# Kernel optimization log

Hardware: AMD Instinct MI355X
Metric: run time of the kernel (lower is better)

The kernel has to match this reference:

```python
import jax, jax.numpy as jnp
import numpy as np

S_IN = 32      # input spatial size
KSZ = 3        # kernel size
STRIDE = 1
S_OUT = (S_IN - KSZ) // STRIDE + 1   # 30
C_IN = 16      # input capsule types
C_OUT = 32     # output capsule types
ROUTINGS = 3
EPS = 1e-7     # K.epsilon()


def _child_parent_map(size_in, size_out, kernel_size):
    # For each parent position, the flat indices of its kernel_size^2 children.
    cpm = np.zeros((size_out ** 2, kernel_size ** 2), dtype=np.int32)
    for p in range(size_out ** 2):
        idx = []
        for kr in range(kernel_size):
            start = kr * size_in + p % size_out + (p // size_out) * size_in
            idx.extend(range(start, start + kernel_size))
        cpm[p] = idx
    return cpm

_CPM = jnp.asarray(_child_parent_map(S_IN, S_OUT, KSZ))  # [S_OUT^2, KSZ^2]


def setup_inputs() -> dict:
    key = jax.random.key(0)
    k1, k2, k3, k4, k5 = jax.random.split(key, 5)
    return {
        "input_act": jax.random.uniform(k1, (S_IN, S_IN, C_IN, 1), dtype=jnp.float32),
        "input_pose": jax.random.normal(k2, (S_IN, S_IN, C_IN, 4, 4), dtype=jnp.float32),
        "transformation_weights": jax.random.normal(k3, (1, KSZ * KSZ * C_IN, C_OUT, 4, 4), dtype=jnp.float32) * 0.1,
        "beta_a": jax.random.normal(k4, (1, 1, C_OUT), dtype=jnp.float32),
        "beta_v": jax.random.normal(k5, (1, 1, C_OUT, 1), dtype=jnp.float32),
    }


def reference(input_act, input_pose, transformation_weights, beta_a, beta_v):
    P = S_OUT ** 2                 # parent positions
    N = KSZ * KSZ * C_IN           # children per parent

    pose = input_pose.reshape(S_IN ** 2, C_IN, 4, 4)
    act = input_act.reshape(S_IN ** 2, C_IN, 1)

    # gather children per parent position (irregular gather via child_parent_map)
    pose_f = pose[_CPM].reshape(P, N, 4, 4)        # [P, N, 4, 4]
    act_f = act[_CPM].reshape(P, N, 1, 1)          # [P, N, 1, 1] (broadcasts over C_OUT)

    W = transformation_weights[0]                  # [N, C_OUT, 4, 4]
    # votes[p,n,c,i,j] = sum_k pose_f[p,n,i,k] * W[n,c,k,j] (avoids K.tile materialization)
    votes = jnp.einsum('pnik,nckj->pncij', pose_f, W).reshape(P, N, C_OUT, 16)

    rr = jnp.full((P, N, C_OUT, 1), 1.0 / C_OUT, dtype=votes.dtype)

    out_act = None
    means = None
    for i in range(ROUTINGS):
        lambd = 0.01 * (1.0 - 0.95 ** i)
        # ---- M step ----
        rs = jnp.sum(rr, axis=1, keepdims=True)                              # [P,1,C,1]
        means = jnp.sum(rr * votes, axis=1, keepdims=True) / rs              # [P,1,C,16]
        var = jnp.sum(rr * jnp.square(votes - means), axis=1, keepdims=True) / rs
        std = jnp.sqrt(var)                                                  # [P,1,C,16]
        costs = beta_v + jnp.log(std + EPS) * rs                             # [P,1,C,16]
        out_act = jax.nn.sigmoid(lambd * (beta_a - jnp.sum(costs, axis=-1)))[..., None]  # [P,1,C,1]
        if i < ROUTINGS - 1:
            # ---- E step ----
            prob_exp = -jnp.sum(jnp.square(votes - means) / (2.0 * jnp.square(std)),
                                axis=-1, keepdims=True)                      # [P,N,C,1]
            prob_main = -jnp.sum(jnp.log(std + EPS), axis=-1, keepdims=True)  # [P,1,C,1]
            zz = jnp.log(out_act + EPS) + prob_main + prob_exp
            rr = jax.nn.softmax(zz, axis=0)                                   # softmax over parent axis, as in source

    out_act = out_act.reshape(S_OUT, S_OUT, C_OUT, 1)
    out_pose = means.reshape(S_OUT, S_OUT, C_OUT, 4, 4)
    return (out_act, out_pose)
```

## Files before the change

### kernel.cpp

```cpp
#include <hip/hip_runtime.h>


#define S_IN   32
#define S_OUT  30
#define PP     (S_OUT * S_OUT)
#define NN     144
#define NREP   16
#define PLSZ   (NN * 32)
#define EPSF   1e-7f
#define CLAMPA 80.0f

#define LOADW(dst, n_) do {                                              \
    const float4* _wp = (const float4*)&W[((n_) * 32 + c) * 16];         \
    float4 _w0 = _wp[0], _w1 = _wp[1], _w2 = _wp[2], _w3 = _wp[3];       \
    dst[0] = _w0.x; dst[1] = _w0.y; dst[2] = _w0.z; dst[3] = _w0.w;      \
    dst[4] = _w1.x; dst[5] = _w1.y; dst[6] = _w1.z; dst[7] = _w1.w;      \
    dst[8] = _w2.x; dst[9] = _w2.y; dst[10] = _w2.z; dst[11] = _w2.w;    \
    dst[12] = _w3.x; dst[13] = _w3.y; dst[14] = _w3.z; dst[15] = _w3.w;  \
} while (0)

#define LOADPO(dst, n_) do {                                             \
    const float4* _pp = (const float4*)&pose_s[(n_) * 16];               \
    float4 _p0 = _pp[0], _p1 = _pp[1], _p2 = _pp[2], _p3 = _pp[3];       \
    dst[0] = _p0.x; dst[1] = _p0.y; dst[2] = _p0.z; dst[3] = _p0.w;      \
    dst[4] = _p1.x; dst[5] = _p1.y; dst[6] = _p1.z; dst[7] = _p1.w;      \
    dst[8] = _p2.x; dst[9] = _p2.y; dst[10] = _p2.z; dst[11] = _p2.w;    \
    dst[12] = _p3.x; dst[13] = _p3.y; dst[14] = _p3.z; dst[15] = _p3.w;  \
} while (0)

#define VOTES(v_, po_, w_) do {                                          \
    _Pragma("unroll")                                                    \
    for (int _i = 0; _i < 4; ++_i) {                                     \
        float _p0 = po_[_i*4+0], _p1 = po_[_i*4+1];                      \
        float _p2 = po_[_i*4+2], _p3 = po_[_i*4+3];                      \
        _Pragma("unroll")                                                \
        for (int _j = 0; _j < 4; ++_j)                                   \
            v_[_i*4+_j] = fmaf(_p0, w_[_j], fmaf(_p1, w_[4+_j],          \
                          fmaf(_p2, w_[8+_j], _p3 * w_[12+_j])));        \
    }                                                                    \
} while (0)

template <bool FIRST, bool LAST>
__global__ __launch_bounds__(512, 4) void me_kernel(
    const float* __restrict__ pose,
    const float* __restrict__ W,
    const float* __restrict__ beta_a,
    const float* __restrict__ beta_v,
    const float* __restrict__ csC,
    float* __restrict__ csW,
    float* __restrict__ meanw,
    float* __restrict__ i2vw,
    float* __restrict__ basew,
    float* __restrict__ out,
    float lambd)
{
    const int p = blockIdx.x;
    const int t = threadIdx.x;
    const int c = t & 31;
    const int slot = t >> 5;
    const int wave = t >> 6;
    const int rep = p & (NREP - 1);

    __shared__ float pose_s[NN * 16];
    __shared__ float red[33 * 8 * 32];
    __shared__ float mean_s[16 * 32];
    __shared__ float i2v_s[16 * 32];
    __shared__ float base_s[32];
    __shared__ float lg[4 * 32];

    const int prow = p / S_OUT, pcol = p % S_OUT;
    {
        const float4* pose4 = (const float4*)pose;
        float4* ps4 = (float4*)pose_s;
        for (int idx = t; idx < 576; idx += 512) {
            int kk = idx >> 6;
            int child = (prow + kk / 3) * S_IN + (pcol + kk % 3);
            ps4[idx] = pose4[child * 64 + (idx & 63)];
        }
    }

    float mn[16], iv[16], base = 0.f;
    if (!FIRST) {
        const float4* m4 = (const float4*)&meanw[(p * 32 + c) * 16];
        const float4* v4 = (const float4*)&i2vw[(p * 32 + c) * 16];
#pragma unroll
        for (int q = 0; q < 4; ++q) {
            float4 a = m4[q], b = v4[q];
            mn[q * 4 + 0] = a.x; mn[q * 4 + 1] = a.y; mn[q * 4 + 2] = a.z; mn[q * 4 + 3] = a.w;
            iv[q * 4 + 0] = b.x; iv[q * 4 + 1] = b.y; iv[q * 4 + 2] = b.z; iv[q * 4 + 3] = b.w;
        }
        base = basew[p * 32 + c];
    }
    __syncthreads();

    float rsum = 0.f;
    float s1[16], s2[16];
#pragma unroll
    for (int q = 0; q < 16; ++q) { s1[q] = 0.f; s2[q] = 0.f; }

    float w[16];
    LOADW(w, slot);
    float cs = 1.f;
    if (!FIRST) cs = csC[slot * 32 + c];

    for (int k = 0; k < 9; ++k) {
        const int n = (k << 4) + slot;
        float po[16];
        LOADPO(po, n);
        float v[16];
        VOTES(v, po, w);
        float cs_next = cs;
        if (k < 8) {
            LOADW(w, n + 16);
            if (!FIRST) cs_next = csC[(n + 16) * 32 + c];
        }
        if (FIRST) {
#pragma unroll
            for (int q = 0; q < 16; ++q) {
                s1[q] += v[q];
                s2[q] = fmaf(v[q], v[q], s2[q]);
            }
        } else {
            float pe = 0.f;
#pragma unroll
            for (int q = 0; q < 16; ++q) {
                float d = v[q] - mn[q];
                pe = fmaf(d * d, iv[q], pe);
            }
            float r = __expf(fminf(base - pe, CLAMPA)) * __builtin_amdgcn_rcpf(cs);
#pragma unroll
            for (int q = 0; q < 16; ++q) {
                s1[q] = fmaf(r, v[q], s1[q]);
                float rv = r * v[q];
                s2[q] = fmaf(rv, v[q], s2[q]);
            }
            rsum += r;
        }
        cs = cs_next;
    }

#pragma unroll
    for (int q = 0; q < 16; ++q) {
        s1[q] += __shfl_xor(s1[q], 32);
        s2[q] += __shfl_xor(s2[q], 32);
    }
    rsum += __shfl_xor(rsum, 32);

    if ((t & 32) == 0) {
#pragma unroll
        for (int q = 0; q < 16; ++q) {
            red[(q * 8 + wave) * 32 + c] = s1[q];
            red[((16 + q) * 8 + wave) * 32 + c] = s2[q];
        }
        red[(32 * 8 + wave) * 32 + c] = rsum;
    }
    __syncthreads();

    if (t < 128) {
        const int qq = t >> 5, cl = t & 31;
        float rs, inv_rs;
        if (FIRST) {
            rs = 4.5f;
            inv_rs = 1.0f / 144.0f;
        } else {
            rs = 0.f;
#pragma unroll
            for (int w8 = 0; w8 < 8; ++w8) rs += red[(32 * 8 + w8) * 32 + cl];
            inv_rs = 1.0f / rs;
        }
        float lsum = 0.f;
        float mq[4], vq[4];
#pragma unroll
        for (int u = 0; u < 4; ++u) {
            const int q = qq * 4 + u;
            float a1 = 0.f, a2 = 0.f;
#pragma unroll
            for (int w8 = 0; w8 < 8; ++w8) {
                a1 += red[(q * 8 + w8) * 32 + cl];
                a2 += red[((16 + q) * 8 + w8) * 32 + cl];
            }
            float m = a1 * inv_rs;
            float var = fmaxf(a2 * inv_rs - m * m, 1e-30f);
            float sd = __builtin_sqrtf(var);
            mq[u] = m;
            vq[u] = 0.5f / var;
            lsum += __logf(sd + EPSF);
            mean_s[q * 32 + cl] = m;
            i2v_s[q * 32 + cl] = vq[u];
        }
        lg[qq * 32 + cl] = lsum;
        float4 mv; mv.x = mq[0]; mv.y = mq[1]; mv.z = mq[2]; mv.w = mq[3];
        if (LAST) {
            ((float4*)(out + PP * 32))[(p * 32 + cl) * 4 + qq] = mv;
        } else {
            float4 vv; vv.x = vq[0]; vv.y = vq[1]; vv.z = vq[2]; vv.w = vq[3];
            ((float4*)meanw)[(p * 32 + cl) * 4 + qq] = mv;
            ((float4*)i2vw)[(p * 32 + cl) * 4 + qq] = vv;
        }
    }
    __syncthreads();

    if (t < 32) {
        float rs;
        if (FIRST) {
            rs = 4.5f;
        } else {
            rs = 0.f;
#pragma unroll
            for (int w8 = 0; w8 < 8; ++w8) rs += red[(32 * 8 + w8) * 32 + c];
        }
        float lsum = lg[c] + lg[32 + c] + lg[64 + c] + lg[96 + c];
        float sumcosts = 16.f * beta_v[c] + rs * lsum;
        float a = 1.0f / (1.0f + __expf(-(lambd * (beta_a[c] - sumcosts))));
        if (LAST) {
            out[p * 32 + c] = a;
        } else {
            float b = __logf(a + EPSF) - lsum;
            basew[p * 32 + c] = b;
            base_s[c] = b;
        }
    }

    if (!LAST) {
        __syncthreads();
        float tbase = base_s[c];
#pragma unroll
        for (int q = 0; q < 16; ++q) {
            mn[q] = mean_s[q * 32 + c];
            iv[q] = i2v_s[q * 32 + c];
        }
        LOADW(w, slot);
        float* csp = csW + rep * PLSZ;
        for (int k = 0; k < 9; ++k) {
            const int n = (k << 4) + slot;
            float po[16];
            LOADPO(po, n);
            float v[16];
            VOTES(v, po, w);
            if (k < 8) LOADW(w, n + 16);
            float pe = 0.f;
#pragma unroll
            for (int q = 0; q < 16; ++q) {
                float d = v[q] - mn[q];
                pe = fmaf(d * d, iv[q], pe);
            }
            float e = __expf(fminf(tbase - pe, CLAMPA));
            atomicAdd(&csp[n * 32 + c], e);
        }
    }
}

__global__ __launch_bounds__(256) void collapse_kernel(
    const float* __restrict__ planes, float* __restrict__ csum)
{
    const int idx = blockIdx.x * 256 + threadIdx.x;
    if (idx >= PLSZ) return;
    float s0 = 0.f, s1 = 0.f, s2 = 0.f, s3 = 0.f;
#pragma unroll
    for (int r = 0; r < NREP; r += 4) {
        s0 += planes[(r + 0) * PLSZ + idx];
        s1 += planes[(r + 1) * PLSZ + idx];
        s2 += planes[(r + 2) * PLSZ + idx];
        s3 += planes[(r + 3) * PLSZ + idx];
    }
    csum[idx] = (s0 + s1) + (s2 + s3);
}

extern "C" void kernel_launch(void* const* d_in, const int* in_sizes, int n_in,
                              void* d_out, int out_size, void* d_ws, size_t ws_size,
                              hipStream_t stream) {
    const float* pose   = (const float*)d_in[1];
    const float* W      = (const float*)d_in[2];
    const float* beta_a = (const float*)d_in[3];
    const float* beta_v = (const float*)d_in[4];
    float* out = (float*)d_out;
    float* ws = (float*)d_ws;

    float* meanw   = ws;
    float* i2vw    = meanw + PP * 32 * 16;
    float* basew   = i2vw + PP * 32 * 16;
    float* planes0 = basew + PP * 32;
    float* planes1 = planes0 + NREP * PLSZ;
    float* csum0   = planes1 + NREP * PLSZ;
    float* csum1   = csum0 + PLSZ;

    const float lambd0 = 0.0f;
    const float lambd1 = 0.01f * (1.0f - 0.95f);
    const float lambd2 = 0.01f * (1.0f - 0.95f * 0.95f);

    const int cg = (PLSZ + 255) / 256;

    hipMemsetAsync(planes0, 0, 2 * NREP * PLSZ * sizeof(float), stream);

    me_kernel<true, false><<<PP, 512, 0, stream>>>(
        pose, W, beta_a, beta_v, csum0, planes0, meanw, i2vw, basew, out, lambd0);
    collapse_kernel<<<cg, 256, 0, stream>>>(planes0, csum0);
    me_kernel<false, false><<<PP, 512, 0, stream>>>(
        pose, W, beta_a, beta_v, csum0, planes1, meanw, i2vw, basew, out, lambd1);
    collapse_kernel<<<cg, 256, 0, stream>>>(planes1, csum1);
    me_kernel<false, true><<<PP, 512, 0, stream>>>(
        pose, W, beta_a, beta_v, csum1, nullptr, meanw, i2vw, basew, out, lambd2);
}
```

Measured before the change: 122.7 us.

## Process two horizontally adjacent parents per block to share weight loads

Each block now handles two neighbouring parent positions (pA, pA+1). It loads a 3x4 child window into shared memory and reuses each transformation-weight register load for both parents' votes. The aim is to halve per-parent weight traffic and block count and to cut launch and sync overhead per parent. In exchange, register pressure roughly doubles: launch bounds drop to 2 blocks per SM, loops are fully unrolled, and the stats and base phases run serially for the two parents.

```diff
diff --git a/kernel.cpp b/kernel.cpp
--- a/kernel.cpp
+++ b/kernel.cpp
@@ -7,6 +7,7 @@
 #define NN     144
 #define NREP   16
 #define PLSZ   (NN * 32)
+#define NBLK   (PP / 2)
 #define EPSF   1e-7f
 #define CLAMPA 80.0f
 
@@ -19,8 +20,8 @@
     dst[12] = _w3.x; dst[13] = _w3.y; dst[14] = _w3.z; dst[15] = _w3.w;  \
 } while (0)
 
-#define LOADPO(dst, n_) do {                                             \
-    const float4* _pp = (const float4*)&pose_s[(n_) * 16];               \
+#define LOADPO(dst, row_) do {                                           \
+    const float4* _pp = (const float4*)&pose_s[(row_) * 16];             \
     float4 _p0 = _pp[0], _p1 = _pp[1], _p2 = _pp[2], _p3 = _pp[3];       \
     dst[0] = _p0.x; dst[1] = _p0.y; dst[2] = _p0.z; dst[3] = _p0.w;      \
     dst[4] = _p1.x; dst[5] = _p1.y; dst[6] = _p1.z; dst[7] = _p1.w;      \
@@ -40,8 +41,118 @@
     }                                                                    \
 } while (0)
 
+#define PE(pe_, v_, mn_, iv_) float pe_;                                 \
+    do {                                                                 \
+        float _a = 0.f, _b = 0.f;                                        \
+        _Pragma("unroll")                                                \
+        for (int _q = 0; _q < 16; _q += 2) {                             \
+            float _d0 = v_[_q] - mn_[_q];                                \
+            float _d1 = v_[_q+1] - mn_[_q+1];                            \
+            _a = fmaf(_d0 * _d0, iv_[_q], _a);                           \
+            _b = fmaf(_d1 * _d1, iv_[_q+1], _b);                         \
+        }                                                                \
+        pe_ = _a + _b;                                                   \
+    } while (0)
+
+#define LOADSTATS(mn_, iv_, p_) do {                                     \
+    const float4* _m4 = (const float4*)&meanw[((p_) * 32 + c) * 16];     \
+    const float4* _v4 = (const float4*)&i2vw[((p_) * 32 + c) * 16];      \
+    _Pragma("unroll")                                                    \
+    for (int _q = 0; _q < 4; ++_q) {                                     \
+        float4 _a = _m4[_q], _b = _v4[_q];                               \
+        mn_[_q*4+0] = _a.x; mn_[_q*4+1] = _a.y;                          \
+        mn_[_q*4+2] = _a.z; mn_[_q*4+3] = _a.w;                          \
+        iv_[_q*4+0] = _b.x; iv_[_q*4+1] = _b.y;                          \
+        iv_[_q*4+2] = _b.z; iv_[_q*4+3] = _b.w;                          \
+    }                                                                    \
+} while (0)
+
+#define WRITE_RED(S1, S2, RS) do {                                       \
+    if ((t & 32) == 0) {                                                 \
+        _Pragma("unroll")                                                \
+        for (int q = 0; q < 16; ++q) {                                   \
+            red[(q * 8 + wave) * 32 + c] = S1[q];                        \
+            red[((16 + q) * 8 + wave) * 32 + c] = S2[q];                 \
+        }                                                                \
+        red[(32 * 8 + wave) * 32 + c] = RS;                              \
+    }                                                                    \
+} while (0)
+
+__constant__ int UA_TAB[9] = {0, 1, 2, 4, 5, 6, 8, 9, 10};
+
 template <bool FIRST, bool LAST>
-__global__ __launch_bounds__(512, 4) void me_kernel(
+__device__ __forceinline__ void stats_phase(
+    const float* __restrict__ red, float* lg, float* rs_s,
+    float* mean_sp, float* i2v_sp,
+    float* __restrict__ meanw, float* __restrict__ i2vw,
+    float* __restrict__ out, int p, int t)
+{
+    if (t < 128) {
+        const int qq = t >> 5, cl = t & 31;
+        float rs, inv_rs;
+        if (FIRST) { rs = 4.5f; inv_rs = 1.0f / 144.0f; }
+        else {
+            rs = 0.f;
+#pragma unroll
+            for (int w8 = 0; w8 < 8; ++w8) rs += red[(32 * 8 + w8) * 32 + cl];
+            inv_rs = 1.0f / rs;
+        }
+        if (qq == 0) rs_s[cl] = rs;
+        float lsum = 0.f;
+        float mq[4], vq[4];
+#pragma unroll
+        for (int u = 0; u < 4; ++u) {
+            const int q = qq * 4 + u;
+            float a1 = 0.f, a2 = 0.f;
+#pragma unroll
+            for (int w8 = 0; w8 < 8; ++w8) {
+                a1 += red[(q * 8 + w8) * 32 + cl];
+                a2 += red[((16 + q) * 8 + w8) * 32 + cl];
+            }
+            float m = a1 * inv_rs;
+            float var = fmaxf(a2 * inv_rs - m * m, 1e-30f);
+            float sd = __builtin_sqrtf(var);
+            mq[u] = m; vq[u] = 0.5f / var;
+            lsum += __logf(sd + EPSF);
+            mean_sp[q * 32 + cl] = m;
+            i2v_sp[q * 32 + cl] = vq[u];
+        }
+        lg[qq * 32 + cl] = lsum;
+        float4 mv; mv.x = mq[0]; mv.y = mq[1]; mv.z = mq[2]; mv.w = mq[3];
+        if (LAST) {
+            ((float4*)(out + PP * 32))[(p * 32 + cl) * 4 + qq] = mv;
+        } else {
+            float4 vv; vv.x = vq[0]; vv.y = vq[1]; vv.z = vq[2]; vv.w = vq[3];
+            ((float4*)meanw)[(p * 32 + cl) * 4 + qq] = mv;
+            ((float4*)i2vw)[(p * 32 + cl) * 4 + qq] = vv;
+        }
+    }
+}
+
+template <bool FIRST, bool LAST>
+__device__ __forceinline__ void base_phase(
+    const float* lg, const float* rs_s, float* base_sp,
+    const float* __restrict__ beta_a, const float* __restrict__ beta_v,
+    float* __restrict__ basew, float* __restrict__ out, int p, int t, float lambd)
+{
+    if (t < 32) {
+        const int c = t;
+        float rs = FIRST ? 4.5f : rs_s[c];
+        float lsum = lg[c] + lg[32 + c] + lg[64 + c] + lg[96 + c];
+        float sumcosts = 16.f * beta_v[c] + rs * lsum;
+        float a = 1.0f / (1.0f + __expf(-(lambd * (beta_a[c] - sumcosts))));
+        if (LAST) {
+            out[p * 32 + c] = a;
+        } else {
+            float b = __logf(a + EPSF) - lsum;
+            basew[p * 32 + c] = b;
+            base_sp[c] = b;
+        }
+    }
+}
+
+template <bool FIRST, bool LAST>
+__global__ __launch_bounds__(512, 2) void me_kernel(
     const float* __restrict__ pose,
     const float* __restrict__ W,
     const float* __restrict__ beta_a,
@@ -54,198 +165,146 @@
     float* __restrict__ out,
     float lambd)
 {
-    const int p = blockIdx.x;
+    const int b = blockIdx.x;
+    const int pA = 2 * b, pB = 2 * b + 1;
     const int t = threadIdx.x;
     const int c = t & 31;
     const int slot = t >> 5;
     const int wave = t >> 6;
-    const int rep = p & (NREP - 1);
-
-    __shared__ float pose_s[NN * 16];
+
+    __shared__ float pose_s[12 * 16 * 16];
     __shared__ float red[33 * 8 * 32];
-    __shared__ float mean_s[16 * 32];
-    __shared__ float i2v_s[16 * 32];
-    __shared__ float base_s[32];
+    __shared__ float mean_s[2][16 * 32];
+    __shared__ float i2v_s[2][16 * 32];
+    __shared__ float base_s[2][32];
+    __shared__ float rs_s[2][32];
     __shared__ float lg[4 * 32];
 
-    const int prow = p / S_OUT, pcol = p % S_OUT;
+    const int rowA = pA / S_OUT, colA = pA % S_OUT;
     {
         const float4* pose4 = (const float4*)pose;
         float4* ps4 = (float4*)pose_s;
-        for (int idx = t; idx < 576; idx += 512) {
-            int kk = idx >> 6;
-            int child = (prow + kk / 3) * S_IN + (pcol + kk % 3);
+        for (int idx = t; idx < 768; idx += 512) {
+            int u = idx >> 6;
+            int child = (rowA + (u >> 2)) * S_IN + (colA + (u & 3));
             ps4[idx] = pose4[child * 64 + (idx & 63)];
         }
     }
 
-    float mn[16], iv[16], base = 0.f;
+    float mnA[16], ivA[16], mnB[16], ivB[16], baseA = 0.f, baseB = 0.f;
     if (!FIRST) {
-        const float4* m4 = (const float4*)&meanw[(p * 32 + c) * 16];
-        const float4* v4 = (const float4*)&i2vw[(p * 32 + c) * 16];
-#pragma unroll
-        for (int q = 0; q < 4; ++q) {
-            float4 a = m4[q], b = v4[q];
-            mn[q * 4 + 0] = a.x; mn[q * 4 + 1] = a.y; mn[q * 4 + 2] = a.z; mn[q * 4 + 3] = a.w;
-            iv[q * 4 + 0] = b.x; iv[q * 4 + 1] = b.y; iv[q * 4 + 2] = b.z; iv[q * 4 + 3] = b.w;
-        }
-        base = basew[p * 32 + c];
-    }
-    __syncthreads();
-
-    float rsum = 0.f;
-    float s1[16], s2[16];
-#pragma unroll
-    for (int q = 0; q < 16; ++q) { s1[q] = 0.f; s2[q] = 0.f; }
+        LOADSTATS(mnA, ivA, pA);
+        LOADSTATS(mnB, ivB, pB);
+        baseA = basew[pA * 32 + c];
+        baseB = basew[pB * 32 + c];
+    }
+    __syncthreads();
+
+    float rsumA = 0.f, rsumB = 0.f;
+    float s1A[16], s2A[16], s1B[16], s2B[16];
+#pragma unroll
+    for (int q = 0; q < 16; ++q) {
+        s1A[q] = 0.f; s2A[q] = 0.f; s1B[q] = 0.f; s2B[q] = 0.f;
+    }
 
     float w[16];
     LOADW(w, slot);
     float cs = 1.f;
     if (!FIRST) cs = csC[slot * 32 + c];
 
+#pragma unroll
     for (int k = 0; k < 9; ++k) {
         const int n = (k << 4) + slot;
-        float po[16];
-        LOADPO(po, n);
-        float v[16];
-        VOTES(v, po, w);
-        float cs_next = cs;
+        const int uA = UA_TAB[k];
+        float poA[16]; LOADPO(poA, uA * 16 + slot);
+        float vA[16];  VOTES(vA, poA, w);
+        float poB[16]; LOADPO(poB, (uA + 1) * 16 + slot);
+        float vB[16];  VOTES(vB, poB, w);
+        const float csq = cs;
         if (k < 8) {
             LOADW(w, n + 16);
-            if (!FIRST) cs_next = csC[(n + 16) * 32 + c];
+            if (!FIRST) cs = csC[(n + 16) * 32 + c];
         }
         if (FIRST) {
 #pragma unroll
             for (int q = 0; q < 16; ++q) {
-                s1[q] += v[q];
-                s2[q] = fmaf(v[q], v[q], s2[q]);
+                s1A[q] += vA[q];
+                s2A[q] = fmaf(vA[q], vA[q], s2A[q]);
+                s1B[q] += vB[q];
+                s2B[q] = fmaf(vB[q], vB[q], s2B[q]);
             }
         } else {
-            float pe = 0.f;
+            PE(peA, vA, mnA, ivA);
+            PE(peB, vB, mnB, ivB);
+            const float inv_cs = __builtin_amdgcn_rcpf(csq);
+            float rA = __expf(fminf(baseA - peA, CLAMPA)) * inv_cs;
+            float rB = __expf(fminf(baseB - peB, CLAMPA)) * inv_cs;
 #pragma unroll
             for (int q = 0; q < 16; ++q) {
-                float d = v[q] - mn[q];
-                pe = fmaf(d * d, iv[q], pe);
+                s1A[q] = fmaf(rA, vA[q], s1A[q]);
+                s2A[q] = fmaf(rA * vA[q], vA[q], s2A[q]);
+                s1B[q] = fmaf(rB, vB[q], s1B[q]);
+                s2B[q] = fmaf(rB * vB[q], vB[q], s2B[q]);
             }
-            float r = __expf(fminf(base - pe, CLAMPA)) * __builtin_amdgcn_rcpf(cs);
-#pragma unroll
-            for (int q = 0; q < 16; ++q) {
-                s1[q] = fmaf(r, v[q], s1[q]);
-                float rv = r * v[q];
-                s2[q] = fmaf(rv, v[q], s2[q]);
-            }
-            rsum += r;
-        }
-        cs = cs_next;
+            rsumA += rA;
+            rsumB += rB;
+        }
     }
 
 #pragma unroll
     for (int q = 0; q < 16; ++q) {
-        s1[q] += __shfl_xor(s1[q], 32);
-        s2[q] += __shfl_xor(s2[q], 32);
-    }
-    rsum += __shfl_xor(rsum, 32);
-
-    if ((t & 32) == 0) {
-#pragma unroll
-        for (int q = 0; q < 16; ++q) {
-            red[(q * 8 + wave) * 32 + c] = s1[q];
-            red[((16 + q) * 8 + wave) * 32 + c] = s2[q];
-        }
-        red[(32 * 8 + wave) * 32 + c] = rsum;
-    }
-    __syncthreads();
-
-    if (t < 128) {
-        const int qq = t >> 5, cl = t & 31;
-        float rs, inv_rs;
-        if (FIRST) {
-            rs = 4.5f;
-            inv_rs = 1.0f / 144.0f;
-        } else {
-            rs = 0.f;
-#pragma unroll
-            for (int w8 = 0; w8 < 8; ++w8) rs += red[(32 * 8 + w8) * 32 + cl];
-            inv_rs = 1.0f / rs;
-        }
-        float lsum = 0.f;
-        float mq[4], vq[4];
-#pragma unroll
-        for (int u = 0; u < 4; ++u) {
-            const int q = qq * 4 + u;
-            float a1 = 0.f, a2 = 0.f;
-#pragma unroll
-            for (int w8 = 0; w8 < 8; ++w8) {
-                a1 += red[(q * 8 + w8) * 32 + cl];
-                a2 += red[((16 + q) * 8 + w8) * 32 + cl];
-            }
-            float m = a1 * inv_rs;
-            float var = fmaxf(a2 * inv_rs - m * m, 1e-30f);
-            float sd = __builtin_sqrtf(var);
-            mq[u] = m;
-            vq[u] = 0.5f / var;
-            lsum += __logf(sd + EPSF);
-            mean_s[q * 32 + cl] = m;
-            i2v_s[q * 32 + cl] = vq[u];
-        }
-        lg[qq * 32 + cl] = lsum;
-        float4 mv; mv.x = mq[0]; mv.y = mq[1]; mv.z = mq[2]; mv.w = mq[3];
-        if (LAST) {
-            ((float4*)(out + PP * 32))[(p * 32 + cl) * 4 + qq] = mv;
-        } else {
-            float4 vv; vv.x = vq[0]; vv.y = vq[1]; vv.z = vq[2]; vv.w = vq[3];
-            ((float4*)meanw)[(p * 32 + cl) * 4 + qq] = mv;
-            ((float4*)i2vw)[(p * 32 + cl) * 4 + qq] = vv;
-        }
-    }
-    __syncthreads();
-
-    if (t < 32) {
-        float rs;
-        if (FIRST) {
-            rs = 4.5f;
-        } else {
-            rs = 0.f;
-#pragma unroll
-            for (int w8 = 0; w8 < 8; ++w8) rs += red[(32 * 8 + w8) * 32 + c];
-        }
-        float lsum = lg[c] + lg[32 + c] + lg[64 + c] + lg[96 + c];
-        float sumcosts = 16.f * beta_v[c] + rs * lsum;
-        float a = 1.0f / (1.0f + __expf(-(lambd * (beta_a[c] - sumcosts))));
-        if (LAST) {
-            out[p * 32 + c] = a;
-        } else {
-            float b = __logf(a + EPSF) - lsum;
-            basew[p * 32 + c] = b;
-            base_s[c] = b;
-        }
-    }
+        s1A[q] += __shfl_xor(s1A[q], 32);
+        s2A[q] += __shfl_xor(s2A[q], 32);
+        s1B[q] += __shfl_xor(s1B[q], 32);
+        s2B[q] += __shfl_xor(s2B[q], 32);
+    }
+    rsumA += __shfl_xor(rsumA, 32);
+    rsumB += __shfl_xor(rsumB, 32);
+
+    WRITE_RED(s1A, s2A, rsumA);
+    __syncthreads();
+    stats_phase<FIRST, LAST>(red, lg, rs_s[0], mean_s[0], i2v_s[0],
+                             meanw, i2vw, out, pA, t);
+    __syncthreads();
+    base_phase<FIRST, LAST>(lg, rs_s[0], base_s[0], beta_a, beta_v,
+                            basew, out, pA, t, lambd);
+    WRITE_RED(s1B, s2B, rsumB);
+    __syncthreads();
+    stats_phase<FIRST, LAST>(red, lg, rs_s[1], mean_s[1], i2v_s[1],
+                             meanw, i2vw, out, pB, t);
+    __syncthreads();
+    base_phase<FIRST, LAST>(lg, rs_s[1], base_s[1], beta_a, beta_v,
+                            basew, out, pB, t, lambd);
 
     if (!LAST) {
         __syncthreads();
-        float tbase = base_s[c];
 #pragma unroll
         for (int q = 0; q < 16; ++q) {
-            mn[q] = mean_s[q * 32 + c];
-            iv[q] = i2v_s[q * 32 + c];
-        }
+            mnA[q] = mean_s[0][q * 32 + c];
+            ivA[q] = i2v_s[0][q * 32 + c];
+            mnB[q] = mean_s[1][q * 32 + c];
+            ivB[q] = i2v_s[1][q * 32 + c];
+        }
+        const float bA = base_s[0][c];
+        const float bB = base_s[1][c];
         LOADW(w, slot);
-        float* csp = csW + rep * PLSZ;
+        float* cspA = csW + (pA & (NREP - 1)) * PLSZ;
+        float* cspB = csW + (pB & (NREP - 1)) * PLSZ;
+#pragma unroll
         for (int k = 0; k < 9; ++k) {
             const int n = (k << 4) + slot;
-            float po[16];
-            LOADPO(po, n);
-            float v[16];
-            VOTES(v, po, w);
+            const int uA = UA_TAB[k];
+            float poA[16]; LOADPO(poA, uA * 16 + slot);
+            float vA[16];  VOTES(vA, poA, w);
+            float poB[16]; LOADPO(poB, (uA + 1) * 16 + slot);
+            float vB[16];  VOTES(vB, poB, w);
             if (k < 8) LOADW(w, n + 16);
-            float pe = 0.f;
-#pragma unroll
-            for (int q = 0; q < 16; ++q) {
-                float d = v[q] - mn[q];
-                pe = fmaf(d * d, iv[q], pe);
-            }
-            float e = __expf(fminf(tbase - pe, CLAMPA));
-            atomicAdd(&csp[n * 32 + c], e);
+            PE(peA, vA, mnA, ivA);
+            PE(peB, vB, mnB, ivB);
+            float eA = __expf(fminf(bA - peA, CLAMPA));
+            float eB = __expf(fminf(bB - peB, CLAMPA));
+            atomicAdd(&cspA[n * 32 + c], eA);
+            atomicAdd(&cspB[n * 32 + c], eB);
         }
     }
 }
@@ -292,12 +351,12 @@
 
     hipMemsetAsync(planes0, 0, 2 * NREP * PLSZ * sizeof(float), stream);
 
-    me_kernel<true, false><<<PP, 512, 0, stream>>>(
+    me_kernel<true, false><<<NBLK, 512, 0, stream>>>(
         pose, W, beta_a, beta_v, csum0, planes0, meanw, i2vw, basew, out, lambd0);
     collapse_kernel<<<cg, 256, 0, stream>>>(planes0, csum0);
-    me_kernel<false, false><<<PP, 512, 0, stream>>>(
+    me_kernel<false, false><<<NBLK, 512, 0, stream>>>(
         pose, W, beta_a, beta_v, csum0, planes1, meanw, i2vw, basew, out, lambd1);
     collapse_kernel<<<cg, 256, 0, stream>>>(planes1, csum1);
-    me_kernel<false, true><<<PP, 512, 0, stream>>>(
+    me_kernel<false, true><<<NBLK, 512, 0, stream>>>(
         pose, W, beta_a, beta_v, csum1, nullptr, meanw, i2vw, basew, out, lambd2);
 }
```

New measurement: 129.4 us. 5.5% more time.

## Expand Gaussian exponent algebraically and split reduction to cut shared memory

Applied to the files above, without the earlier changes.

Rewrites the per-vote exponent sum (v-m)^2*iv as v*(iv*v - 2*iv*m) plus a constant folded into the base term. This trims the subtraction per component and uses two independent accumulators. The block reduction now handles s1 and s2 in two passes over a smaller shared buffer, with all 512 threads finishing one component each. The k loops are fully unrolled. The changes aim to lower ALU work, shared-memory footprint and occupancy pressure, at the cost of extra barriers, scalar global stores and possible loss of precision from cancellation in the expanded quadratic.

```diff
diff --git a/kernel.cpp b/kernel.cpp
--- a/kernel.cpp
+++ b/kernel.cpp
@@ -39,6 +39,19 @@
                           fmaf(_p2, w_[8+_j], _p3 * w_[12+_j])));        \
     }                                                                    \
 } while (0)
+
+#define PEQ(pe_, v_, iv_, m2b_) float pe_;                               \
+    do {                                                                 \
+        float _a = 0.f, _b = 0.f;                                        \
+        _Pragma("unroll")                                                \
+        for (int _q = 0; _q < 16; _q += 2) {                             \
+            float _t0 = fmaf(iv_[_q], v_[_q], m2b_[_q]);                 \
+            float _t1 = fmaf(iv_[_q+1], v_[_q+1], m2b_[_q+1]);           \
+            _a = fmaf(v_[_q], _t0, _a);                                  \
+            _b = fmaf(v_[_q+1], _t1, _b);                                \
+        }                                                                \
+        pe_ = _a + _b;                                                   \
+    } while (0)
 
 template <bool FIRST, bool LAST>
 __global__ __launch_bounds__(512, 4) void me_kernel(
@@ -59,14 +72,16 @@
     const int c = t & 31;
     const int slot = t >> 5;
     const int wave = t >> 6;
-    const int rep = p & (NREP - 1);
 
     __shared__ float pose_s[NN * 16];
-    __shared__ float red[33 * 8 * 32];
+    __shared__ float red[16 * 8 * 32];
+    __shared__ float rsum_s[8 * 32];
     __shared__ float mean_s[16 * 32];
-    __shared__ float i2v_s[16 * 32];
-    __shared__ float base_s[32];
-    __shared__ float lg[4 * 32];
+    __shared__ float iv_s[16 * 32];
+    __shared__ float m2b_s[16 * 32];
+    __shared__ float logstd_s[16 * 32];
+    __shared__ float rs_s[32];
+    __shared__ float bstar_s[32];
 
     const int prow = p / S_OUT, pcol = p % S_OUT;
     {
@@ -79,17 +94,26 @@
         }
     }
 
-    float mn[16], iv[16], base = 0.f;
+    float iv[16], m2b[16], bstar = 0.f;
     if (!FIRST) {
+        float cst = 0.f;
         const float4* m4 = (const float4*)&meanw[(p * 32 + c) * 16];
         const float4* v4 = (const float4*)&i2vw[(p * 32 + c) * 16];
 #pragma unroll
-        for (int q = 0; q < 4; ++q) {
-            float4 a = m4[q], b = v4[q];
-            mn[q * 4 + 0] = a.x; mn[q * 4 + 1] = a.y; mn[q * 4 + 2] = a.z; mn[q * 4 + 3] = a.w;
-            iv[q * 4 + 0] = b.x; iv[q * 4 + 1] = b.y; iv[q * 4 + 2] = b.z; iv[q * 4 + 3] = b.w;
-        }
-        base = basew[p * 32 + c];
+        for (int q4 = 0; q4 < 4; ++q4) {
+            float4 a = m4[q4], b = v4[q4];
+            float mq[4] = {a.x, a.y, a.z, a.w};
+            float vq[4] = {b.x, b.y, b.z, b.w};
+#pragma unroll
+            for (int u = 0; u < 4; ++u) {
+                int q = q4 * 4 + u;
+                iv[q] = vq[u];
+                float tq = vq[u] * mq[u];
+                m2b[q] = -2.f * tq;
+                cst = fmaf(tq, mq[u], cst);
+            }
+        }
+        bstar = basew[p * 32 + c] - cst;
     }
     __syncthreads();
 
@@ -103,16 +127,17 @@
     float cs = 1.f;
     if (!FIRST) cs = csC[slot * 32 + c];
 
+#pragma unroll
     for (int k = 0; k < 9; ++k) {
         const int n = (k << 4) + slot;
         float po[16];
         LOADPO(po, n);
         float v[16];
         VOTES(v, po, w);
-        float cs_next = cs;
+        const float csq = cs;
         if (k < 8) {
             LOADW(w, n + 16);
-            if (!FIRST) cs_next = csC[(n + 16) * 32 + c];
+            if (!FIRST) cs = csC[(n + 16) * 32 + c];
         }
         if (FIRST) {
 #pragma unroll
@@ -121,22 +146,15 @@
                 s2[q] = fmaf(v[q], v[q], s2[q]);
             }
         } else {
-            float pe = 0.f;
-#pragma unroll
-            for (int q = 0; q < 16; ++q) {
-                float d = v[q] - mn[q];
-                pe = fmaf(d * d, iv[q], pe);
-            }
-            float r = __expf(fminf(base - pe, CLAMPA)) * __builtin_amdgcn_rcpf(cs);
+            PEQ(pe, v, iv, m2b);
+            float r = __expf(fminf(bstar - pe, CLAMPA)) * __builtin_amdgcn_rcpf(csq);
 #pragma unroll
             for (int q = 0; q < 16; ++q) {
                 s1[q] = fmaf(r, v[q], s1[q]);
-                float rv = r * v[q];
-                s2[q] = fmaf(rv, v[q], s2[q]);
+                s2[q] = fmaf(r * v[q], v[q], s2[q]);
             }
             rsum += r;
         }
-        cs = cs_next;
     }
 
 #pragma unroll
@@ -148,68 +166,62 @@
 
     if ((t & 32) == 0) {
 #pragma unroll
-        for (int q = 0; q < 16; ++q) {
-            red[(q * 8 + wave) * 32 + c] = s1[q];
-            red[((16 + q) * 8 + wave) * 32 + c] = s2[q];
-        }
-        red[(32 * 8 + wave) * 32 + c] = rsum;
-    }
-    __syncthreads();
-
-    if (t < 128) {
-        const int qq = t >> 5, cl = t & 31;
+        for (int q = 0; q < 16; ++q) red[(q * 8 + wave) * 32 + c] = s1[q];
+        rsum_s[wave * 32 + c] = rsum;
+    }
+    __syncthreads();
+
+    {
+        const int q = slot;
+        float a1 = 0.f;
+#pragma unroll
+        for (int w8 = 0; w8 < 8; ++w8) a1 += red[(q * 8 + w8) * 32 + c];
         float rs, inv_rs;
-        if (FIRST) {
-            rs = 4.5f;
-            inv_rs = 1.0f / 144.0f;
-        } else {
+        if (FIRST) { rs = 4.5f; inv_rs = 1.0f / 144.0f; }
+        else {
             rs = 0.f;
 #pragma unroll
-            for (int w8 = 0; w8 < 8; ++w8) rs += red[(32 * 8 + w8) * 32 + cl];
+            for (int w8 = 0; w8 < 8; ++w8) rs += rsum_s[w8 * 32 + c];
             inv_rs = 1.0f / rs;
         }
+        float mean = a1 * inv_rs;
+        mean_s[q * 32 + c] = mean;
+        if (q == 0) rs_s[c] = rs;
+        if (LAST) out[PP * 32 + (p * 32 + c) * 16 + q] = mean;
+        else      meanw[(p * 32 + c) * 16 + q] = mean;
+    }
+    __syncthreads();
+
+    if ((t & 32) == 0) {
+#pragma unroll
+        for (int q = 0; q < 16; ++q) red[(q * 8 + wave) * 32 + c] = s2[q];
+    }
+    __syncthreads();
+
+    {
+        const int q = slot;
+        float a2 = 0.f;
+#pragma unroll
+        for (int w8 = 0; w8 < 8; ++w8) a2 += red[(q * 8 + w8) * 32 + c];
+        float inv_rs = FIRST ? (1.0f / 144.0f) : (1.0f / rs_s[c]);
+        float mean = mean_s[q * 32 + c];
+        float var = fmaxf(a2 * inv_rs - mean * mean, 1e-30f);
+        float sd = __builtin_sqrtf(var);
+        logstd_s[q * 32 + c] = __logf(sd + EPSF);
+        if (!LAST) {
+            float ivv = 0.5f / var;
+            iv_s[q * 32 + c] = ivv;
+            m2b_s[q * 32 + c] = -2.f * ivv * mean;
+            i2vw[(p * 32 + c) * 16 + q] = ivv;
+        }
+    }
+    __syncthreads();
+
+    if (t < 32) {
+        float rs = FIRST ? 4.5f : rs_s[c];
         float lsum = 0.f;
-        float mq[4], vq[4];
-#pragma unroll
-        for (int u = 0; u < 4; ++u) {
-            const int q = qq * 4 + u;
-            float a1 = 0.f, a2 = 0.f;
-#pragma unroll
-            for (int w8 = 0; w8 < 8; ++w8) {
-                a1 += red[(q * 8 + w8) * 32 + cl];
-                a2 += red[((16 + q) * 8 + w8) * 32 + cl];
-            }
-            float m = a1 * inv_rs;
-            float var = fmaxf(a2 * inv_rs - m * m, 1e-30f);
-            float sd = __builtin_sqrtf(var);
-            mq[u] = m;
-            vq[u] = 0.5f / var;
-            lsum += __logf(sd + EPSF);
-            mean_s[q * 32 + cl] = m;
-            i2v_s[q * 32 + cl] = vq[u];
-        }
-        lg[qq * 32 + cl] = lsum;
-        float4 mv; mv.x = mq[0]; mv.y = mq[1]; mv.z = mq[2]; mv.w = mq[3];
-        if (LAST) {
-            ((float4*)(out + PP * 32))[(p * 32 + cl) * 4 + qq] = mv;
-        } else {
-            float4 vv; vv.x = vq[0]; vv.y = vq[1]; vv.z = vq[2]; vv.w = vq[3];
-            ((float4*)meanw)[(p * 32 + cl) * 4 + qq] = mv;
-            ((float4*)i2vw)[(p * 32 + cl) * 4 + qq] = vv;
-        }
-    }
-    __syncthreads();
-
-    if (t < 32) {
-        float rs;
-        if (FIRST) {
-            rs = 4.5f;
-        } else {
-            rs = 0.f;
-#pragma unroll
-            for (int w8 = 0; w8 < 8; ++w8) rs += red[(32 * 8 + w8) * 32 + c];
-        }
-        float lsum = lg[c] + lg[32 + c] + lg[64 + c] + lg[96 + c];
+#pragma unroll
+        for (int q = 0; q < 16; ++q) lsum += logstd_s[q * 32 + c];
         float sumcosts = 16.f * beta_v[c] + rs * lsum;
         float a = 1.0f / (1.0f + __expf(-(lambd * (beta_a[c] - sumcosts))));
         if (LAST) {
@@ -217,20 +229,27 @@
         } else {
             float b = __logf(a + EPSF) - lsum;
             basew[p * 32 + c] = b;
-            base_s[c] = b;
+            float cst = 0.f;
+#pragma unroll
+            for (int q = 0; q < 16; ++q) {
+                float m = mean_s[q * 32 + c];
+                cst = fmaf(iv_s[q * 32 + c] * m, m, cst);
+            }
+            bstar_s[c] = b - cst;
         }
     }
 
     if (!LAST) {
         __syncthreads();
-        float tbase = base_s[c];
 #pragma unroll
         for (int q = 0; q < 16; ++q) {
-            mn[q] = mean_s[q * 32 + c];
-            iv[q] = i2v_s[q * 32 + c];
-        }
+            iv[q] = iv_s[q * 32 + c];
+            m2b[q] = m2b_s[q * 32 + c];
+        }
+        const float bst = bstar_s[c];
         LOADW(w, slot);
-        float* csp = csW + rep * PLSZ;
+        float* csp = csW + (p & (NREP - 1)) * PLSZ;
+#pragma unroll
         for (int k = 0; k < 9; ++k) {
             const int n = (k << 4) + slot;
             float po[16];
@@ -238,13 +257,8 @@
             float v[16];
             VOTES(v, po, w);
             if (k < 8) LOADW(w, n + 16);
-            float pe = 0.f;
-#pragma unroll
-            for (int q = 0; q < 16; ++q) {
-                float d = v[q] - mn[q];
-                pe = fmaf(d * d, iv[q], pe);
-            }
-            float e = __expf(fminf(tbase - pe, CLAMPA));
+            PEQ(pe, v, iv, m2b);
+            float e = __expf(fminf(bst - pe, CLAMPA));
             atomicAdd(&csp[n * 32 + c], e);
         }
     }
```

Result: slower. 138.9 us (+13.2%).

## Replace atomic softmax-denominator accumulation with per-parent planes and two-stage reduction

Applied to the files above, without the earlier changes.

Each parent block now writes its exp terms to its own plane with plain stores instead of doing atomicAdd into 16 replicated planes. The planes are then summed by a two-stage reduction (20 chunks, then a final pass), which also removes the memset. This is meant to eliminate atomic contention and the memset, but it writes and reads about 16.6 MB of planes per routing iteration and adds an extra kernel launch. A small register tweak in the cs prefetch is included.

```diff
diff --git a/kernel.cpp b/kernel.cpp
--- a/kernel.cpp
+++ b/kernel.cpp
@@ -5,8 +5,9 @@
 #define S_OUT  30
 #define PP     (S_OUT * S_OUT)
 #define NN     144
-#define NREP   16
 #define PLSZ   (NN * 32)
+#define NCH    20
+#define CHP    (PP / NCH)
 #define EPSF   1e-7f
 #define CLAMPA 80.0f
 
@@ -47,7 +48,7 @@
     const float* __restrict__ beta_a,
     const float* __restrict__ beta_v,
     const float* __restrict__ csC,
-    float* __restrict__ csW,
+    float* __restrict__ planes,
     float* __restrict__ meanw,
     float* __restrict__ i2vw,
     float* __restrict__ basew,
@@ -59,7 +60,6 @@
     const int c = t & 31;
     const int slot = t >> 5;
     const int wave = t >> 6;
-    const int rep = p & (NREP - 1);
 
     __shared__ float pose_s[NN * 16];
     __shared__ float red[33 * 8 * 32];
@@ -109,10 +109,10 @@
         LOADPO(po, n);
         float v[16];
         VOTES(v, po, w);
-        float cs_next = cs;
+        const float csq = cs;
         if (k < 8) {
             LOADW(w, n + 16);
-            if (!FIRST) cs_next = csC[(n + 16) * 32 + c];
+            if (!FIRST) cs = csC[(n + 16) * 32 + c];
         }
         if (FIRST) {
 #pragma unroll
@@ -127,16 +127,14 @@
                 float d = v[q] - mn[q];
                 pe = fmaf(d * d, iv[q], pe);
             }
-            float r = __expf(fminf(base - pe, CLAMPA)) * __builtin_amdgcn_rcpf(cs);
+            float r = __expf(fminf(base - pe, CLAMPA)) * __builtin_amdgcn_rcpf(csq);
 #pragma unroll
             for (int q = 0; q < 16; ++q) {
                 s1[q] = fmaf(r, v[q], s1[q]);
-                float rv = r * v[q];
-                s2[q] = fmaf(rv, v[q], s2[q]);
+                s2[q] = fmaf(r * v[q], v[q], s2[q]);
             }
             rsum += r;
         }
-        cs = cs_next;
     }
 
 #pragma unroll
@@ -230,7 +228,7 @@
             iv[q] = i2v_s[q * 32 + c];
         }
         LOADW(w, slot);
-        float* csp = csW + rep * PLSZ;
+        float* csp = planes + p * PLSZ;
         for (int k = 0; k < 9; ++k) {
             const int n = (k << 4) + slot;
             float po[16];
@@ -245,25 +243,47 @@
                 pe = fmaf(d * d, iv[q], pe);
             }
             float e = __expf(fminf(tbase - pe, CLAMPA));
-            atomicAdd(&csp[n * 32 + c], e);
+            csp[n * 32 + c] = e;
         }
     }
 }
 
-__global__ __launch_bounds__(256) void collapse_kernel(
-    const float* __restrict__ planes, float* __restrict__ csum)
+__global__ __launch_bounds__(256) void collapse_a(
+    const float* __restrict__ planes, float* __restrict__ partial)
+{
+    const int b = blockIdx.x;
+    const int ch = b / 18;
+    const int idx = (b % 18) * 256 + threadIdx.x;
+    const float* src = planes + ch * CHP * PLSZ + idx;
+    float a0 = 0.f, a1 = 0.f, a2 = 0.f, a3 = 0.f;
+#pragma unroll
+    for (int o = 0; o < CHP; o += 4) {
+        if (o + 3 < CHP) {
+            a0 += src[(o + 0) * PLSZ];
+            a1 += src[(o + 1) * PLSZ];
+            a2 += src[(o + 2) * PLSZ];
+            a3 += src[(o + 3) * PLSZ];
+        } else {
+            for (int u = o; u < CHP; ++u) a0 += src[u * PLSZ];
+        }
+    }
+    partial[ch * PLSZ + idx] = (a0 + a1) + (a2 + a3);
+}
+
+__global__ __launch_bounds__(256) void collapse_b(
+    const float* __restrict__ partial, float* __restrict__ csum)
 {
     const int idx = blockIdx.x * 256 + threadIdx.x;
     if (idx >= PLSZ) return;
-    float s0 = 0.f, s1 = 0.f, s2 = 0.f, s3 = 0.f;
-#pragma unroll
-    for (int r = 0; r < NREP; r += 4) {
-        s0 += planes[(r + 0) * PLSZ + idx];
-        s1 += planes[(r + 1) * PLSZ + idx];
-        s2 += planes[(r + 2) * PLSZ + idx];
-        s3 += planes[(r + 3) * PLSZ + idx];
-    }
-    csum[idx] = (s0 + s1) + (s2 + s3);
+    float a0 = 0.f, a1 = 0.f, a2 = 0.f, a3 = 0.f;
+#pragma unroll
+    for (int ch = 0; ch < NCH; ch += 4) {
+        a0 += partial[(ch + 0) * PLSZ + idx];
+        a1 += partial[(ch + 1) * PLSZ + idx];
+        a2 += partial[(ch + 2) * PLSZ + idx];
+        a3 += partial[(ch + 3) * PLSZ + idx];
+    }
+    csum[idx] = (a0 + a1) + (a2 + a3);
 }
 
 extern "C" void kernel_launch(void* const* d_in, const int* in_sizes, int n_in,
@@ -279,25 +299,26 @@
     float* meanw   = ws;
     float* i2vw    = meanw + PP * 32 * 16;
     float* basew   = i2vw + PP * 32 * 16;
-    float* planes0 = basew + PP * 32;
-    float* planes1 = planes0 + NREP * PLSZ;
-    float* csum0   = planes1 + NREP * PLSZ;
+    float* planes  = basew + PP * 32;
+    float* partial = planes + PP * PLSZ;
+    float* csum0   = partial + NCH * PLSZ;
     float* csum1   = csum0 + PLSZ;
 
     const float lambd0 = 0.0f;
     const float lambd1 = 0.01f * (1.0f - 0.95f);
     const float lambd2 = 0.01f * (1.0f - 0.95f * 0.95f);
 
-    const int cg = (PLSZ + 255) / 256;
-
-    hipMemsetAsync(planes0, 0, 2 * NREP * PLSZ * sizeof(float), stream);
+    const int cga = NCH * 18;
+    const int cgb = (PLSZ + 255) / 256;
 
     me_kernel<true, false><<<PP, 512, 0, stream>>>(
-        pose, W, beta_a, beta_v, csum0, planes0, meanw, i2vw, basew, out, lambd0);
-    collapse_kernel<<<cg, 256, 0, stream>>>(planes0, csum0);
+        pose, W, beta_a, beta_v, csum0, planes, meanw, i2vw, basew, out, lambd0);
+    collapse_a<<<cga, 256, 0, stream>>>(planes, partial);
+    collapse_b<<<cgb, 256, 0, stream>>>(partial, csum0);
     me_kernel<false, false><<<PP, 512, 0, stream>>>(
-        pose, W, beta_a, beta_v, csum0, planes1, meanw, i2vw, basew, out, lambd1);
-    collapse_kernel<<<cg, 256, 0, stream>>>(planes1, csum1);
+        pose, W, beta_a, beta_v, csum0, planes, meanw, i2vw, basew, out, lambd1);
+    collapse_a<<<cga, 256, 0, stream>>>(planes, partial);
+    collapse_b<<<cgb, 256, 0, stream>>>(partial, csum1);
     me_kernel<false, true><<<PP, 512, 0, stream>>>(
         pose, W, beta_a, beta_v, csum1, nullptr, meanw, i2vw, basew, out, lambd2);
 }
```

Measured after the change: 129.4 us. 5.5% more time.
